# Optimization experiments

Measured on AMD Instinct MI355X. Metric: run time of the kernel, lower is better.

## Reference

```python
import jax, jax.numpy as jnp
import numpy as np

HEADS = 8
DIM_HEAD = 64


def setup_inputs() -> dict:
    key = jax.random.key(0)
    ks = jax.random.split(key, 9)
    b, n, d = 2, 2048, 512
    inner = HEADS * DIM_HEAD  # 512
    s = 0.02
    return {
        "x": jax.random.normal(ks[0], (b, n, d), dtype=jnp.float32),
        "attn_bias": jax.random.normal(ks[1], (1, HEADS, n, n), dtype=jnp.float32),
        "Wq": jax.random.normal(ks[2], (d, inner), dtype=jnp.float32) * s,
        "Wkv": jax.random.normal(ks[3], (d, 2 * inner), dtype=jnp.float32) * s,
        "Wo": jax.random.normal(ks[4], (inner, d), dtype=jnp.float32) * s,
        "bo": jax.random.normal(ks[5], (d,), dtype=jnp.float32) * s,
        "Wg": jax.random.normal(ks[6], (d, inner), dtype=jnp.float32) * s,
        "bg": jnp.ones((inner,), dtype=jnp.float32),
    }


def reference(x, attn_bias, Wq, Wkv, Wo, bo, Wg, bg):
    b, n, d = x.shape
    h, dh = HEADS, DIM_HEAD
    scale = dh ** -0.5
    # projections: [b, n, h*dh] -> [b, h, n, dh]
    q = (x @ Wq).reshape(b, n, h, dh).transpose(0, 2, 1, 3) * scale
    k, v = jnp.split(x @ Wkv, 2, axis=-1)
    k = k.reshape(b, n, h, dh).transpose(0, 2, 1, 3)
    v = v.reshape(b, n, h, dh).transpose(0, 2, 1, 3)
    # scores + additive bias; max-subtract softmax (stable, as in original)
    dots = jnp.einsum('bhid,bhjd->bhij', q, k) + attn_bias
    attn = jax.nn.softmax(dots, axis=-1)
    out = jnp.einsum('bhij,bhjd->bhid', attn, v)
    out = out.transpose(0, 2, 1, 3).reshape(b, n, h * dh)
    # gating sigmoid epilogue
    gates = jax.nn.sigmoid(x @ Wg + bg)
    out = out * gates
    return out @ Wo + bo
```

## Files before the change

### kernel.cpp

```cpp
#include <hip/hip_runtime.h>
#include <hip/hip_bf16.h>

typedef __bf16 bf16_t;
typedef __bf16 bf16x8 __attribute__((ext_vector_type(8)));
typedef float f32x4 __attribute__((ext_vector_type(4)));

static __device__ __forceinline__ bf16_t to_bf16(float f) { return (bf16_t)f; }

__global__ void k_convert_x(const float* __restrict__ src, bf16_t* __restrict__ dst, int n8) {
  int i = blockIdx.x * blockDim.x + threadIdx.x;
  if (i >= n8) return;
  const float4* s = reinterpret_cast<const float4*>(src) + (size_t)i * 2;
  float4 a = s[0], b = s[1];
  bf16x8 v;
  v[0]=(bf16_t)a.x; v[1]=(bf16_t)a.y; v[2]=(bf16_t)a.z; v[3]=(bf16_t)a.w;
  v[4]=(bf16_t)b.x; v[5]=(bf16_t)b.y; v[6]=(bf16_t)b.z; v[7]=(bf16_t)b.w;
  reinterpret_cast<bf16x8*>(dst)[i] = v;
}

__global__ void k_transpose_cvt(const float* __restrict__ src, bf16_t* __restrict__ dst, int Nc) {
  __shared__ bf16_t tile[64 * 72];
  const int n0 = blockIdx.x * 64, k0 = blockIdx.y * 64;
  const int t = threadIdx.x;
  #pragma unroll
  for (int it = 0; it < 16; ++it) {
    int c = t + it * 256;
    int kl = c >> 6, nl = c & 63;
    tile[kl * 72 + nl] = to_bf16(src[(size_t)(k0 + kl) * Nc + n0 + nl]);
  }
  __syncthreads();
  #pragma unroll
  for (int it = 0; it < 16; ++it) {
    int c = t + it * 256;
    int nl = c >> 6, kl = c & 63;
    dst[(size_t)(n0 + nl) * 512 + k0 + kl] = tile[kl * 72 + nl];
  }
}

__global__ __launch_bounds__(256) void k_gemm_proj(
    const bf16_t* __restrict__ A,
    const bf16_t* __restrict__ BT,
    const float*  __restrict__ bg,
    bf16_t* __restrict__ qo,
    bf16_t* __restrict__ ko,
    bf16_t* __restrict__ vto,
    float*  __restrict__ go)
{
  __shared__ __align__(16) bf16_t lA[128 * 72];
  __shared__ __align__(16) bf16_t lB[128 * 72];
  const int t = threadIdx.x;
  const int w = t >> 6, lane = t & 63, lr = lane & 15, lg = lane >> 4;
  const int wr = w >> 1, wc = w & 1;
  const int m0 = blockIdx.y * 128, n0 = blockIdx.x * 128;
  f32x4 acc[4][4] = {};
  for (int k0 = 0; k0 < 512; k0 += 64) {
    __syncthreads();
    #pragma unroll
    for (int it = 0; it < 4; ++it) {
      int c = t + it * 256;
      int row = c >> 3, cc = c & 7;
      *reinterpret_cast<bf16x8*>(&lA[row * 72 + cc * 8]) =
          *reinterpret_cast<const bf16x8*>(&A[(size_t)(m0 + row) * 512 + k0 + cc * 8]);
      *reinterpret_cast<bf16x8*>(&lB[row * 72 + cc * 8]) =
          *reinterpret_cast<const bf16x8*>(&BT[(size_t)(n0 + row) * 512 + k0 + cc * 8]);
    }
    __syncthreads();
    #pragma unroll
    for (int kk = 0; kk < 2; ++kk) {
      bf16x8 af[4], bfm[4];
      #pragma unroll
      for (int mf = 0; mf < 4; ++mf)
        af[mf] = *reinterpret_cast<const bf16x8*>(&lA[(wr*64 + mf*16 + lr) * 72 + kk*32 + lg*8]);
      #pragma unroll
      for (int nf = 0; nf < 4; ++nf)
        bfm[nf] = *reinterpret_cast<const bf16x8*>(&lB[(wc*64 + nf*16 + lr) * 72 + kk*32 + lg*8]);
      #pragma unroll
      for (int mf = 0; mf < 4; ++mf)
        #pragma unroll
        for (int nf = 0; nf < 4; ++nf)
          acc[mf][nf] = __builtin_amdgcn_mfma_f32_16x16x32_bf16(af[mf], bfm[nf], acc[mf][nf], 0, 0, 0);
    }
  }
  const int seg = n0 >> 9;
  #pragma unroll
  for (int mf = 0; mf < 4; ++mf) {
    #pragma unroll
    for (int nf = 0; nf < 4; ++nf) {
      #pragma unroll
      for (int r = 0; r < 4; ++r) {
        int rm = m0 + wr*64 + mf*16 + lg*4 + r;
        int cn = n0 + wc*64 + nf*16 + lr;
        float v = acc[mf][nf][r];
        int b = rm >> 11, n = rm & 2047;
        int c = cn & 511;
        if (seg == 0) {
          int h = c >> 6, dh = c & 63;
          qo[((size_t)(b*8 + h) * 2048 + n) * 64 + dh] = to_bf16(v * 0.125f);
        } else if (seg == 1) {
          int h = c >> 6, dh = c & 63;
          ko[((size_t)(b*8 + h) * 2048 + n) * 64 + dh] = to_bf16(v);
        } else if (seg == 2) {
          int h = c >> 6, dh = c & 63;
          vto[((size_t)(b*8 + h) * 64 + dh) * 2048 + n] = to_bf16(v);
        } else {
          float z = v + bg[c];
          go[(size_t)rm * 512 + c] = 1.0f / (1.0f + __expf(-z));
        }
      }
    }
  }
}

template<int FINAL>
__global__ __launch_bounds__(256, 4) void k_attn(
    const bf16_t* __restrict__ q,
    const bf16_t* __restrict__ kb,
    const bf16_t* __restrict__ vt,
    const float*  __restrict__ bias,
    const float*  __restrict__ gates,
    bf16_t* __restrict__ ao,
    float* __restrict__ pO,
    float* __restrict__ pm,
    float* __restrict__ pl)
{
  __shared__ __align__(16) bf16_t lK[64 * 72];
  __shared__ __align__(16) bf16_t lV[64 * 72];
  __shared__ __align__(16) bf16_t lP[4][16 * 72];
  const int t = threadIdx.x, w = t >> 6, lane = t & 63, lr = lane & 15, lg = lane >> 4;
  const int bh = blockIdx.y, b = bh >> 3, h = bh & 7;
  const int i0 = blockIdx.x * 64, ib = i0 + w * 16;
  const int ntile = 32 / (int)gridDim.z;
  const int sz = blockIdx.z;
  const int jbase = sz * ntile * 64;

  bf16x8 aq[2];
  const bf16_t* qp = q + ((size_t)bh * 2048 + ib + lr) * 64;
  aq[0] = *reinterpret_cast<const bf16x8*>(qp + lg * 8);
  aq[1] = *reinterpret_cast<const bf16x8*>(qp + 32 + lg * 8);

  float m_r[4] = {-1e30f, -1e30f, -1e30f, -1e30f};
  float l_r[4] = {0.f, 0.f, 0.f, 0.f};
  f32x4 accO[4] = {};

  const float* bias_p = bias + (size_t)h * 2048 * 2048 + (size_t)(ib + lg * 4) * 2048 + lr;
  const bf16_t* kp = kb + (size_t)bh * 2048 * 64;
  const bf16_t* vp = vt + (size_t)bh * 64 * 2048;

  const int srow = t >> 3, scc = t & 7;
  const int srow1 = (t + 256) >> 3;

  bf16x8 rK0, rK1, rV0, rV1;
  float bv[4][4];
  {
    const int j0 = jbase;
    rK0 = *reinterpret_cast<const bf16x8*>(&kp[(size_t)(j0 + srow)  * 64 + scc * 8]);
    rK1 = *reinterpret_cast<const bf16x8*>(&kp[(size_t)(j0 + srow1) * 64 + scc * 8]);
    rV0 = *reinterpret_cast<const bf16x8*>(&vp[(size_t)srow  * 2048 + j0 + scc * 8]);
    rV1 = *reinterpret_cast<const bf16x8*>(&vp[(size_t)srow1 * 2048 + j0 + scc * 8]);
    #pragma unroll
    for (int nf = 0; nf < 4; ++nf)
      #pragma unroll
      for (int r = 0; r < 4; ++r)
        bv[nf][r] = bias_p[(size_t)r * 2048 + j0 + nf * 16];
  }

  for (int jt = 0; jt < ntile; ++jt) {
    const int j1 = jbase + (jt + 1) * 64;
    const bool more = (jt + 1 < ntile);

    __syncthreads();
    *reinterpret_cast<bf16x8*>(&lK[srow  * 72 + scc * 8]) = rK0;
    *reinterpret_cast<bf16x8*>(&lK[srow1 * 72 + scc * 8]) = rK1;
    *reinterpret_cast<bf16x8*>(&lV[srow  * 72 + scc * 8]) = rV0;
    *reinterpret_cast<bf16x8*>(&lV[srow1 * 72 + scc * 8]) = rV1;
    __syncthreads();

    if (more) {
      rK0 = *reinterpret_cast<const bf16x8*>(&kp[(size_t)(j1 + srow)  * 64 + scc * 8]);
      rK1 = *reinterpret_cast<const bf16x8*>(&kp[(size_t)(j1 + srow1) * 64 + scc * 8]);
      rV0 = *reinterpret_cast<const bf16x8*>(&vp[(size_t)srow  * 2048 + j1 + scc * 8]);
      rV1 = *reinterpret_cast<const bf16x8*>(&vp[(size_t)srow1 * 2048 + j1 + scc * 8]);
    }

    f32x4 s[4] = {};
    #pragma unroll
    for (int kk = 0; kk < 2; ++kk) {
      #pragma unroll
      for (int nf = 0; nf < 4; ++nf) {
        bf16x8 bf = *reinterpret_cast<const bf16x8*>(&lK[(nf*16 + lr) * 72 + kk*32 + lg*8]);
        s[nf] = __builtin_amdgcn_mfma_f32_16x16x32_bf16(aq[kk], bf, s[nf], 0, 0, 0);
      }
    }
    #pragma unroll
    for (int nf = 0; nf < 4; ++nf)
      #pragma unroll
      for (int r = 0; r < 4; ++r)
        s[nf][r] += bv[nf][r];
    if (more) {
      #pragma unroll
      for (int nf = 0; nf < 4; ++nf)
        #pragma unroll
        for (int r = 0; r < 4; ++r)
          bv[nf][r] = bias_p[(size_t)r * 2048 + j1 + nf * 16];
    }

    #pragma unroll
    for (int r = 0; r < 4; ++r) {
      float rmx = fmaxf(fmaxf(s[0][r], s[1][r]), fmaxf(s[2][r], s[3][r]));
      rmx = fmaxf(rmx, __shfl_xor(rmx, 1));
      rmx = fmaxf(rmx, __shfl_xor(rmx, 2));
      rmx = fmaxf(rmx, __shfl_xor(rmx, 4));
      rmx = fmaxf(rmx, __shfl_xor(rmx, 8));
      float mnew = fmaxf(m_r[r], rmx);
      float corr = __expf(m_r[r] - mnew);
      m_r[r] = mnew;
      float rs = 0.f;
      #pragma unroll
      for (int nf = 0; nf < 4; ++nf) {
        float p = __expf(s[nf][r] - mnew);
        s[nf][r] = p;
        rs += p;
      }
      rs += __shfl_xor(rs, 1); rs += __shfl_xor(rs, 2);
      rs += __shfl_xor(rs, 4); rs += __shfl_xor(rs, 8);
      l_r[r] = l_r[r] * corr + rs;
      #pragma unroll
      for (int df = 0; df < 4; ++df) accO[df][r] *= corr;
    }

    #pragma unroll
    for (int nf = 0; nf < 4; ++nf)
      #pragma unroll
      for (int r = 0; r < 4; ++r)
        lP[w][(lg*4 + r) * 72 + nf*16 + lr] = to_bf16(s[nf][r]);

    #pragma unroll
    for (int kk = 0; kk < 2; ++kk) {
      bf16x8 pa = *reinterpret_cast<const bf16x8*>(&lP[w][lr * 72 + kk*32 + lg*8]);
      #pragma unroll
      for (int df = 0; df < 4; ++df) {
        bf16x8 bv8 = *reinterpret_cast<const bf16x8*>(&lV[(df*16 + lr) * 72 + kk*32 + lg*8]);
        accO[df] = __builtin_amdgcn_mfma_f32_16x16x32_bf16(pa, bv8, accO[df], 0, 0, 0);
      }
    }
  }

  if (FINAL) {
    #pragma unroll
    for (int r = 0; r < 4; ++r) {
      float inv = 1.0f / l_r[r];
      int ig = ib + lg*4 + r;
      #pragma unroll
      for (int df = 0; df < 4; ++df) {
        int dg = h*64 + df*16 + lr;
        float gate = gates[(size_t)(b*2048 + ig) * 512 + dg];
        ao[(size_t)(b*2048 + ig) * 512 + dg] = to_bf16(accO[df][r] * inv * gate);
      }
    }
  } else {
    float* po = pO + (((size_t)sz * 16 + bh) * 2048) * 64;
    #pragma unroll
    for (int r = 0; r < 4; ++r) {
      int ig = ib + lg*4 + r;
      #pragma unroll
      for (int df = 0; df < 4; ++df)
        po[(size_t)ig * 64 + df*16 + lr] = accO[df][r];
    }
    if (lr == 0) {
      size_t rb = ((size_t)sz * 16 + bh) * 2048 + ib + lg*4;
      #pragma unroll
      for (int r = 0; r < 4; ++r) { pm[rb + r] = m_r[r]; pl[rb + r] = l_r[r]; }
    }
  }
}

__global__ __launch_bounds__(256) void k_attn_combine(
    const float* __restrict__ pO, const float* __restrict__ pm, const float* __restrict__ pl,
    const float* __restrict__ gates, bf16_t* __restrict__ ao, int nsplit)
{
  int idx = blockIdx.x * 256 + threadIdx.x;
  int dh = idx & 63, row = (idx >> 6) & 2047, bh = idx >> 17;
  int b = bh >> 3, h = bh & 7;
  const size_t SP_O = (size_t)16 * 2048 * 64, SP_S = (size_t)16 * 2048;
  size_t rb = (size_t)bh * 2048 + row;
  float M = -1e30f;
  for (int s = 0; s < nsplit; ++s) M = fmaxf(M, pm[s * SP_S + rb]);
  float L = 0.f, O = 0.f;
  for (int s = 0; s < nsplit; ++s) {
    float wgt = __expf(pm[s * SP_S + rb] - M);
    L += pl[s * SP_S + rb] * wgt;
    O += pO[s * SP_O + rb * 64 + dh] * wgt;
  }
  float gate = gates[(size_t)(b * 2048 + row) * 512 + h * 64 + dh];
  ao[(size_t)(b * 2048 + row) * 512 + h * 64 + dh] = to_bf16(O / L * gate);
}

__global__ __launch_bounds__(256) void k_gemm_out(
    const bf16_t* __restrict__ A,
    const bf16_t* __restrict__ BT,
    const float*  __restrict__ bo,
    float* __restrict__ out)
{
  __shared__ __align__(16) bf16_t lA[128 * 72];
  __shared__ __align__(16) bf16_t lB[128 * 72];
  const int t = threadIdx.x;
  const int w = t >> 6, lane = t & 63, lr = lane & 15, lg = lane >> 4;
  const int wr = w >> 1, wc = w & 1;
  const int m0 = blockIdx.y * 128, n0 = blockIdx.x * 128;
  f32x4 acc[4][4] = {};
  for (int k0 = 0; k0 < 512; k0 += 64) {
    __syncthreads();
    #pragma unroll
    for (int it = 0; it < 4; ++it) {
      int c = t + it * 256;
      int row = c >> 3, cc = c & 7;
      *reinterpret_cast<bf16x8*>(&lA[row * 72 + cc * 8]) =
          *reinterpret_cast<const bf16x8*>(&A[(size_t)(m0 + row) * 512 + k0 + cc * 8]);
      *reinterpret_cast<bf16x8*>(&lB[row * 72 + cc * 8]) =
          *reinterpret_cast<const bf16x8*>(&BT[(size_t)(n0 + row) * 512 + k0 + cc * 8]);
    }
    __syncthreads();
    #pragma unroll
    for (int kk = 0; kk < 2; ++kk) {
      bf16x8 af[4], bfm[4];
      #pragma unroll
      for (int mf = 0; mf < 4; ++mf)
        af[mf] = *reinterpret_cast<const bf16x8*>(&lA[(wr*64 + mf*16 + lr) * 72 + kk*32 + lg*8]);
      #pragma unroll
      for (int nf = 0; nf < 4; ++nf)
        bfm[nf] = *reinterpret_cast<const bf16x8*>(&lB[(wc*64 + nf*16 + lr) * 72 + kk*32 + lg*8]);
      #pragma unroll
      for (int mf = 0; mf < 4; ++mf)
        #pragma unroll
        for (int nf = 0; nf < 4; ++nf)
          acc[mf][nf] = __builtin_amdgcn_mfma_f32_16x16x32_bf16(af[mf], bfm[nf], acc[mf][nf], 0, 0, 0);
    }
  }
  #pragma unroll
  for (int mf = 0; mf < 4; ++mf) {
    #pragma unroll
    for (int nf = 0; nf < 4; ++nf) {
      #pragma unroll
      for (int r = 0; r < 4; ++r) {
        int rm = m0 + wr*64 + mf*16 + lg*4 + r;
        int cn = n0 + wc*64 + nf*16 + lr;
        out[(size_t)rm * 512 + cn] = acc[mf][nf][r] + bo[cn];
      }
    }
  }
}

extern "C" void kernel_launch(void* const* d_in, const int* in_sizes, int n_in,
                              void* d_out, int out_size, void* d_ws, size_t ws_size,
                              hipStream_t stream) {
  const float* x    = (const float*)d_in[0];
  const float* bias = (const float*)d_in[1];
  const float* Wq   = (const float*)d_in[2];
  const float* Wkv  = (const float*)d_in[3];
  const float* Wo   = (const float*)d_in[4];
  const float* bo   = (const float*)d_in[5];
  const float* Wg   = (const float*)d_in[6];
  const float* bg   = (const float*)d_in[7];
  float* out = (float*)d_out;

  char* ws = (char*)d_ws;
  const size_t MB = 1024 * 1024;
  bf16_t* x_bf  = (bf16_t*)(ws + 0 * MB);
  bf16_t* WcatT = (bf16_t*)(ws + 4 * MB);
  bf16_t* WoT   = (bf16_t*)(ws + 6 * MB);
  bf16_t* q_bf  = (bf16_t*)(ws + 7 * MB);
  bf16_t* k_bf  = (bf16_t*)(ws + 11 * MB);
  bf16_t* vt_bf = (bf16_t*)(ws + 15 * MB);
  float*  g_f32 = (float*) (ws + 19 * MB);
  bf16_t* ao_bf = (bf16_t*)(ws + 27 * MB);
  float*  pO    = (float*) (ws + 31 * MB);
  float*  pm    = (float*) (ws + 47 * MB);
  float*  pl    = (float*) (ws + 47 * MB + 256 * 1024);

  k_convert_x<<<1024, 256, 0, stream>>>(x, x_bf, 2097152 / 8);
  k_transpose_cvt<<<dim3(8, 8),  256, 0, stream>>>(Wq,  WcatT,               512);
  k_transpose_cvt<<<dim3(16, 8), 256, 0, stream>>>(Wkv, WcatT + 512 * 512,  1024);
  k_transpose_cvt<<<dim3(8, 8),  256, 0, stream>>>(Wg,  WcatT + 1536 * 512,  512);
  k_transpose_cvt<<<dim3(8, 8),  256, 0, stream>>>(Wo,  WoT,                 512);
  k_gemm_proj<<<dim3(16, 32), 256, 0, stream>>>(x_bf, WcatT, bg, q_bf, k_bf, vt_bf, g_f32);

  if (ws_size >= 48 * MB) {
    k_attn<0><<<dim3(32, 16, 2), 256, 0, stream>>>(q_bf, k_bf, vt_bf, bias, nullptr,
                                                   nullptr, pO, pm, pl);
    k_attn_combine<<<8192, 256, 0, stream>>>(pO, pm, pl, g_f32, ao_bf, 2);
  } else {
    k_attn<1><<<dim3(32, 16, 1), 256, 0, stream>>>(q_bf, k_bf, vt_bf, bias, g_f32,
                                                   ao_bf, nullptr, nullptr, nullptr);
  }
  k_gemm_out<<<dim3(4, 32), 256, 0, stream>>>(ao_bf, WoT, bo, out);
}
```

Measured before the change: 132.9 us.

## Load K/V MFMA fragments directly from global memory, removing LDS staging

Removes the shared-memory K/V tiles and block-wide barriers; each wave now reads its K and V MFMA operands directly from global memory per tile. The register double-buffered prefetch of the next tile's K, V and bias is dropped, so loads are issued just before use. This cuts LDS traffic and synchronisation but makes four waves redundantly fetch the same K/V data and exposes global load latency, including for the large bias stream.

```diff
diff --git a/kernel.cpp b/kernel.cpp
--- a/kernel.cpp
+++ b/kernel.cpp
@@ -123,8 +123,6 @@
     float* __restrict__ pm,
     float* __restrict__ pl)
 {
-  __shared__ __align__(16) bf16_t lK[64 * 72];
-  __shared__ __align__(16) bf16_t lV[64 * 72];
   __shared__ __align__(16) bf16_t lP[4][16 * 72];
   const int t = threadIdx.x, w = t >> 6, lane = t & 63, lr = lane & 15, lg = lane >> 4;
   const int bh = blockIdx.y, b = bh >> 3, h = bh & 7;
@@ -143,66 +141,47 @@
   f32x4 accO[4] = {};
 
   const float* bias_p = bias + (size_t)h * 2048 * 2048 + (size_t)(ib + lg * 4) * 2048 + lr;
-  const bf16_t* kp = kb + (size_t)bh * 2048 * 64;
-  const bf16_t* vp = vt + (size_t)bh * 64 * 2048;
-
-  const int srow = t >> 3, scc = t & 7;
-  const int srow1 = (t + 256) >> 3;
-
-  bf16x8 rK0, rK1, rV0, rV1;
-  float bv[4][4];
-  {
-    const int j0 = jbase;
-    rK0 = *reinterpret_cast<const bf16x8*>(&kp[(size_t)(j0 + srow)  * 64 + scc * 8]);
-    rK1 = *reinterpret_cast<const bf16x8*>(&kp[(size_t)(j0 + srow1) * 64 + scc * 8]);
-    rV0 = *reinterpret_cast<const bf16x8*>(&vp[(size_t)srow  * 2048 + j0 + scc * 8]);
-    rV1 = *reinterpret_cast<const bf16x8*>(&vp[(size_t)srow1 * 2048 + j0 + scc * 8]);
+  const bf16_t* kfrag = kb + (size_t)bh * 2048 * 64;
+  const bf16_t* vfrag = vt + (size_t)bh * 64 * 2048;
+
+  for (int jt = 0; jt < ntile; ++jt) {
+    const int j0 = jbase + jt * 64;
+
+    bf16x8 kf[2][4];
+    #pragma unroll
+    for (int kk = 0; kk < 2; ++kk)
+      #pragma unroll
+      for (int nf = 0; nf < 4; ++nf)
+        kf[kk][nf] = *reinterpret_cast<const bf16x8*>(
+            &kfrag[(size_t)(j0 + nf*16 + lr) * 64 + kk*32 + lg*8]);
+
+    float bv[4][4];
     #pragma unroll
     for (int nf = 0; nf < 4; ++nf)
       #pragma unroll
       for (int r = 0; r < 4; ++r)
         bv[nf][r] = bias_p[(size_t)r * 2048 + j0 + nf * 16];
-  }
-
-  for (int jt = 0; jt < ntile; ++jt) {
-    const int j1 = jbase + (jt + 1) * 64;
-    const bool more = (jt + 1 < ntile);
-
-    __syncthreads();
-    *reinterpret_cast<bf16x8*>(&lK[srow  * 72 + scc * 8]) = rK0;
-    *reinterpret_cast<bf16x8*>(&lK[srow1 * 72 + scc * 8]) = rK1;
-    *reinterpret_cast<bf16x8*>(&lV[srow  * 72 + scc * 8]) = rV0;
-    *reinterpret_cast<bf16x8*>(&lV[srow1 * 72 + scc * 8]) = rV1;
-    __syncthreads();
-
-    if (more) {
-      rK0 = *reinterpret_cast<const bf16x8*>(&kp[(size_t)(j1 + srow)  * 64 + scc * 8]);
-      rK1 = *reinterpret_cast<const bf16x8*>(&kp[(size_t)(j1 + srow1) * 64 + scc * 8]);
-      rV0 = *reinterpret_cast<const bf16x8*>(&vp[(size_t)srow  * 2048 + j1 + scc * 8]);
-      rV1 = *reinterpret_cast<const bf16x8*>(&vp[(size_t)srow1 * 2048 + j1 + scc * 8]);
-    }
 
     f32x4 s[4] = {};
     #pragma unroll
-    for (int kk = 0; kk < 2; ++kk) {
-      #pragma unroll
-      for (int nf = 0; nf < 4; ++nf) {
-        bf16x8 bf = *reinterpret_cast<const bf16x8*>(&lK[(nf*16 + lr) * 72 + kk*32 + lg*8]);
-        s[nf] = __builtin_amdgcn_mfma_f32_16x16x32_bf16(aq[kk], bf, s[nf], 0, 0, 0);
-      }
-    }
+    for (int kk = 0; kk < 2; ++kk)
+      #pragma unroll
+      for (int nf = 0; nf < 4; ++nf)
+        s[nf] = __builtin_amdgcn_mfma_f32_16x16x32_bf16(aq[kk], kf[kk][nf], s[nf], 0, 0, 0);
+
+    bf16x8 vf[2][4];
+    #pragma unroll
+    for (int kk = 0; kk < 2; ++kk)
+      #pragma unroll
+      for (int df = 0; df < 4; ++df)
+        vf[kk][df] = *reinterpret_cast<const bf16x8*>(
+            &vfrag[(size_t)(df*16 + lr) * 2048 + j0 + kk*32 + lg*8]);
+
     #pragma unroll
     for (int nf = 0; nf < 4; ++nf)
       #pragma unroll
       for (int r = 0; r < 4; ++r)
         s[nf][r] += bv[nf][r];
-    if (more) {
-      #pragma unroll
-      for (int nf = 0; nf < 4; ++nf)
-        #pragma unroll
-        for (int r = 0; r < 4; ++r)
-          bv[nf][r] = bias_p[(size_t)r * 2048 + j1 + nf * 16];
-    }
 
     #pragma unroll
     for (int r = 0; r < 4; ++r) {
@@ -238,10 +217,8 @@
     for (int kk = 0; kk < 2; ++kk) {
       bf16x8 pa = *reinterpret_cast<const bf16x8*>(&lP[w][lr * 72 + kk*32 + lg*8]);
       #pragma unroll
-      for (int df = 0; df < 4; ++df) {
-        bf16x8 bv8 = *reinterpret_cast<const bf16x8*>(&lV[(df*16 + lr) * 72 + kk*32 + lg*8]);
-        accO[df] = __builtin_amdgcn_mfma_f32_16x16x32_bf16(pa, bv8, accO[df], 0, 0, 0);
-      }
+      for (int df = 0; df < 4; ++df)
+        accO[df] = __builtin_amdgcn_mfma_f32_16x16x32_bf16(pa, vf[kk][df], accO[df], 0, 0, 0);
     }
   }
 
```

Measured after the change: 193.7 us. 45.7% more time.
